# Performance work log

Hardware: AMD Instinct MI355X
Metric: run time of the kernel (lower is better)

The kernel has to match this reference:

```python
import jax, jax.numpy as jnp
import numpy as np

B, L, T, H = 8, 16, 1024, 256


def setup_inputs() -> dict:
    key = jax.random.key(0)
    k1, k2 = jax.random.split(key)
    h_blth = jax.random.normal(k1, (B, L, T, H), dtype=jnp.float32)
    # nn.Linear(H, 1): weight [1, H] -> store as [H]; bias [1]
    attn_w = jax.random.normal(k2, (H,), dtype=jnp.float32) / np.sqrt(H)
    attn_b = jnp.zeros((1,), dtype=jnp.float32)
    return {"h_blth": h_blth, "attn_w": attn_w, "attn_b": attn_b}


def reference(h_blth, attn_w, attn_b):
    # scores: [B, L, T]
    s = jnp.einsum('blth,h->blt', h_blth, attn_w) + attn_b[0]
    # global max over T (matches torch .max(dim=2, keepdim=True))
    s_max = jnp.max(s, axis=2, keepdims=True)
    exp_s = jnp.exp(s - s_max)                      # [B, L, T]
    cum_exp = jnp.cumsum(exp_s, axis=2)             # [B, L, T]
    weighted_h = exp_s[..., None] * h_blth          # [B, L, T, H]
    cum_weighted_h = jnp.cumsum(weighted_h, axis=2) # [B, L, T, H]
    ctx = cum_weighted_h / (cum_exp[..., None] + 1e-12)
    return h_blth + ctx
```

## Files before the change

### kernel.cpp

```cpp
#include <hip/hip_runtime.h>


constexpr int Tn = 1024, Hn = 256;
constexpr int BL  = 128;
constexpr int NCH = 8;
constexpr int CT  = Tn / NCH;
constexpr int F4  = Hn / 4;
constexpr int NW  = Tn / 32;

__global__ __launch_bounds__(256) void k_scores(const float* __restrict__ h,
                                                const float* __restrict__ w,
                                                const float* __restrict__ bias,
                                                float* __restrict__ ebuf,
                                                float* __restrict__ P32,
                                                float* __restrict__ Se32) {
    const int wave = threadIdx.x >> 6, lane = threadIdx.x & 63;
    const int g = lane >> 4, sub = lane & 15;
    const int j = blockIdx.x & 7, bl = blockIdx.x >> 3;
    const float b0 = bias[0];
    const float4* wp = reinterpret_cast<const float4*>(w);
    float4 w4[4];
    #pragma unroll
    for (int q = 0; q < 4; ++q) w4[q] = wp[sub + 16 * q];
    const float4* hp = reinterpret_cast<const float4*>(h) + (size_t)bl * Tn * F4;
    const int t0 = j * CT + wave * 32;

    float4 acc[4] = {{0,0,0,0},{0,0,0,0},{0,0,0,0},{0,0,0,0}};
    float esum = 0.f;
    #pragma unroll
    for (int i = 0; i < 8; ++i) {
        const int t = t0 + i * 4 + g;
        float4 x[4];
        #pragma unroll
        for (int q = 0; q < 4; ++q) x[q] = hp[(size_t)t * F4 + sub + 16 * q];
        float p = 0.f;
        #pragma unroll
        for (int q = 0; q < 4; ++q) {
            p = fmaf(x[q].x, w4[q].x, p);
            p = fmaf(x[q].y, w4[q].y, p);
            p = fmaf(x[q].z, w4[q].z, p);
            p = fmaf(x[q].w, w4[q].w, p);
        }
        p += __shfl_xor(p, 1);
        p += __shfl_xor(p, 2);
        p += __shfl_xor(p, 4);
        p += __shfl_xor(p, 8);
        const float e = __expf(p + b0);
        esum += e;
        #pragma unroll
        for (int q = 0; q < 4; ++q) {
            acc[q].x = fmaf(e, x[q].x, acc[q].x);
            acc[q].y = fmaf(e, x[q].y, acc[q].y);
            acc[q].z = fmaf(e, x[q].z, acc[q].z);
            acc[q].w = fmaf(e, x[q].w, acc[q].w);
        }
        if (sub == 0) ebuf[bl * Tn + t] = e;
    }
    #pragma unroll
    for (int q = 0; q < 4; ++q) {
        acc[q].x += __shfl_xor(acc[q].x, 16); acc[q].x += __shfl_xor(acc[q].x, 32);
        acc[q].y += __shfl_xor(acc[q].y, 16); acc[q].y += __shfl_xor(acc[q].y, 32);
        acc[q].z += __shfl_xor(acc[q].z, 16); acc[q].z += __shfl_xor(acc[q].z, 32);
        acc[q].w += __shfl_xor(acc[q].w, 16); acc[q].w += __shfl_xor(acc[q].w, 32);
    }
    esum += __shfl_xor(esum, 16);  esum += __shfl_xor(esum, 32);

    const int W = j * 4 + wave;
    if (lane < 16) {
        float4* pp = reinterpret_cast<float4*>(P32) + ((size_t)bl * NW + W) * F4;
        pp[sub]      = acc[0];
        pp[sub + 16] = acc[1];
        pp[sub + 32] = acc[2];
        pp[sub + 48] = acc[3];
    }
    if (lane == 0) Se32[bl * NW + W] = esum;
}

__global__ __launch_bounds__(256) void k_apply(const float* __restrict__ h,
                                               const float* __restrict__ ebuf,
                                               const float* __restrict__ P32,
                                               const float* __restrict__ Se32,
                                               float* __restrict__ out) {
    const int wave = threadIdx.x >> 6, lane = threadIdx.x & 63;
    const int j = blockIdx.x & 7, bl = blockIdx.x >> 3;
    const int W = j * 4 + wave;
    const int t0 = W * 32;

    const float4* Pp = reinterpret_cast<const float4*>(P32) + (size_t)bl * NW * F4;
    float4 off4 = make_float4(0.f, 0.f, 0.f, 0.f);
    for (int q = 0; q < W; ++q) {
        const float4 v = Pp[q * F4 + lane];
        off4.x += v.x; off4.y += v.y; off4.z += v.z; off4.w += v.w;
    }
    float seo = 0.f;
    if (lane < W) seo = Se32[bl * NW + lane];
    seo += __shfl_xor(seo, 1); seo += __shfl_xor(seo, 2);
    seo += __shfl_xor(seo, 4); seo += __shfl_xor(seo, 8);
    seo += __shfl_xor(seo, 16);
    seo = __shfl(seo, 0);

    float ev = 0.f;
    if (lane < 32) ev = ebuf[bl * Tn + t0 + lane];
    float sc = ev;
    #pragma unroll
    for (int off = 1; off < 32; off <<= 1) {
        const float n = __shfl_up(sc, off);
        if (lane >= off) sc += n;
    }
    const float sdv = 1.0f / (seo + sc + 1e-12f);

    const float4* hp = reinterpret_cast<const float4*>(h)
                       + ((size_t)bl * Tn + t0) * F4 + lane;
    float4* op = reinterpret_cast<float4*>(out)
                 + ((size_t)bl * Tn + t0) * F4 + lane;

    float4 a = off4;
    #pragma unroll
    for (int i = 0; i < 32; i += 8) {
        float4 x[8];
        #pragma unroll
        for (int u = 0; u < 8; ++u) x[u] = hp[(size_t)(i + u) * F4];
        #pragma unroll
        for (int u = 0; u < 8; ++u) {
            const float e = __shfl(ev,  i + u);
            const float s = __shfl(sdv, i + u);
            a.x = fmaf(e, x[u].x, a.x); a.y = fmaf(e, x[u].y, a.y);
            a.z = fmaf(e, x[u].z, a.z); a.w = fmaf(e, x[u].w, a.w);
            float4 o;
            o.x = fmaf(a.x, s, x[u].x); o.y = fmaf(a.y, s, x[u].y);
            o.z = fmaf(a.z, s, x[u].z); o.w = fmaf(a.w, s, x[u].w);
            op[(size_t)(i + u) * F4] = o;
        }
    }
}

extern "C" void kernel_launch(void* const* d_in, const int* in_sizes, int n_in,
                              void* d_out, int out_size, void* d_ws, size_t ws_size,
                              hipStream_t stream) {
    const float* h = (const float*)d_in[0];
    const float* w = (const float*)d_in[1];
    const float* b = (const float*)d_in[2];
    float* out = (float*)d_out;

    float* ebuf = (float*)d_ws;
    float* P32  = ebuf + BL * Tn;
    float* Se32 = P32 + (size_t)BL * NW * Hn;

    k_scores<<<BL * NCH, 256, 0, stream>>>(h, w, b, ebuf, P32, Se32);
    k_apply <<<BL * NCH, 256, 0, stream>>>(h, ebuf, P32, Se32, out);
}
```

Baseline: 262.0 us.

## Fuse score and apply kernels into one cooperative kernel with grid sync

Result: slower. 320.5 us (+22.3%).

```diff
diff --git a/kernel.cpp b/kernel.cpp
--- a/kernel.cpp
+++ b/kernel.cpp
@@ -1,45 +1,44 @@
 #include <hip/hip_runtime.h>
+#include <hip/hip_cooperative_groups.h>
+
+namespace cg = cooperative_groups;
 
 
 constexpr int Tn = 1024, Hn = 256;
 constexpr int BL  = 128;
 constexpr int NCH = 8;
-constexpr int CT  = Tn / NCH;
 constexpr int F4  = Hn / 4;
 constexpr int NW  = Tn / 32;
-
-__global__ __launch_bounds__(256) void k_scores(const float* __restrict__ h,
-                                                const float* __restrict__ w,
-                                                const float* __restrict__ bias,
-                                                float* __restrict__ ebuf,
-                                                float* __restrict__ P32,
-                                                float* __restrict__ Se32) {
-    const int wave = threadIdx.x >> 6, lane = threadIdx.x & 63;
-    const int g = lane >> 4, sub = lane & 15;
-    const int j = blockIdx.x & 7, bl = blockIdx.x >> 3;
-    const float b0 = bias[0];
-    const float4* wp = reinterpret_cast<const float4*>(w);
-    float4 w4[4];
-    #pragma unroll
-    for (int q = 0; q < 4; ++q) w4[q] = wp[sub + 16 * q];
+constexpr int NBLK = 512;
+constexpr int REP  = BL * NCH / NBLK;
+
+__device__ __forceinline__ void phase1_body(int vb, int wave, int lane,
+                                            int g, int sub, float b0,
+                                            const float4* __restrict__ wp4,
+                                            const float* __restrict__ h,
+                                            float* __restrict__ ebuf,
+                                            float* __restrict__ P32,
+                                            float* __restrict__ Se32) {
+    const int j = vb & 7, bl = vb >> 3;
+    const int W = j * 4 + wave;
+    const int t0w = W * 32;
     const float4* hp = reinterpret_cast<const float4*>(h) + (size_t)bl * Tn * F4;
-    const int t0 = j * CT + wave * 32;
 
     float4 acc[4] = {{0,0,0,0},{0,0,0,0},{0,0,0,0},{0,0,0,0}};
     float esum = 0.f;
     #pragma unroll
     for (int i = 0; i < 8; ++i) {
-        const int t = t0 + i * 4 + g;
+        const int t = t0w + i * 4 + g;
         float4 x[4];
         #pragma unroll
         for (int q = 0; q < 4; ++q) x[q] = hp[(size_t)t * F4 + sub + 16 * q];
         float p = 0.f;
         #pragma unroll
         for (int q = 0; q < 4; ++q) {
-            p = fmaf(x[q].x, w4[q].x, p);
-            p = fmaf(x[q].y, w4[q].y, p);
-            p = fmaf(x[q].z, w4[q].z, p);
-            p = fmaf(x[q].w, w4[q].w, p);
+            p = fmaf(x[q].x, wp4[q].x, p);
+            p = fmaf(x[q].y, wp4[q].y, p);
+            p = fmaf(x[q].z, wp4[q].z, p);
+            p = fmaf(x[q].w, wp4[q].w, p);
         }
         p += __shfl_xor(p, 1);
         p += __shfl_xor(p, 2);
@@ -65,7 +64,6 @@
     }
     esum += __shfl_xor(esum, 16);  esum += __shfl_xor(esum, 32);
 
-    const int W = j * 4 + wave;
     if (lane < 16) {
         float4* pp = reinterpret_cast<float4*>(P32) + ((size_t)bl * NW + W) * F4;
         pp[sub]      = acc[0];
@@ -76,15 +74,15 @@
     if (lane == 0) Se32[bl * NW + W] = esum;
 }
 
-__global__ __launch_bounds__(256) void k_apply(const float* __restrict__ h,
-                                               const float* __restrict__ ebuf,
-                                               const float* __restrict__ P32,
-                                               const float* __restrict__ Se32,
-                                               float* __restrict__ out) {
-    const int wave = threadIdx.x >> 6, lane = threadIdx.x & 63;
-    const int j = blockIdx.x & 7, bl = blockIdx.x >> 3;
+__device__ __forceinline__ void phase2_body(int vb, int wave, int lane,
+                                            const float* __restrict__ h,
+                                            const float* __restrict__ ebuf,
+                                            const float* __restrict__ P32,
+                                            const float* __restrict__ Se32,
+                                            float* __restrict__ out) {
+    const int j = vb & 7, bl = vb >> 3;
     const int W = j * 4 + wave;
-    const int t0 = W * 32;
+    const int t0w = W * 32;
 
     const float4* Pp = reinterpret_cast<const float4*>(P32) + (size_t)bl * NW * F4;
     float4 off4 = make_float4(0.f, 0.f, 0.f, 0.f);
@@ -100,7 +98,7 @@
     seo = __shfl(seo, 0);
 
     float ev = 0.f;
-    if (lane < 32) ev = ebuf[bl * Tn + t0 + lane];
+    if (lane < 32) ev = ebuf[bl * Tn + t0w + lane];
     float sc = ev;
     #pragma unroll
     for (int off = 1; off < 32; off <<= 1) {
@@ -110,9 +108,9 @@
     const float sdv = 1.0f / (seo + sc + 1e-12f);
 
     const float4* hp = reinterpret_cast<const float4*>(h)
-                       + ((size_t)bl * Tn + t0) * F4 + lane;
+                       + ((size_t)bl * Tn + t0w) * F4 + lane;
     float4* op = reinterpret_cast<float4*>(out)
-                 + ((size_t)bl * Tn + t0) * F4 + lane;
+                 + ((size_t)bl * Tn + t0w) * F4 + lane;
 
     float4 a = off4;
     #pragma unroll
@@ -134,6 +132,59 @@
     }
 }
 
+__global__ __launch_bounds__(256, 2) void k_coop(const float* __restrict__ h,
+                                                 const float* __restrict__ w,
+                                                 const float* __restrict__ bias,
+                                                 float* __restrict__ ebuf,
+                                                 float* __restrict__ P32,
+                                                 float* __restrict__ Se32,
+                                                 float* __restrict__ out) {
+    const int wave = threadIdx.x >> 6, lane = threadIdx.x & 63;
+    const int g = lane >> 4, sub = lane & 15;
+    const float b0 = bias[0];
+    const float4* wp = reinterpret_cast<const float4*>(w);
+    float4 w4[4];
+    #pragma unroll
+    for (int q = 0; q < 4; ++q) w4[q] = wp[sub + 16 * q];
+
+    #pragma unroll
+    for (int rep = 0; rep < REP; ++rep)
+        phase1_body(blockIdx.x + rep * NBLK, wave, lane, g, sub, b0, w4,
+                    h, ebuf, P32, Se32);
+
+    cg::this_grid().sync();
+
+    #pragma unroll
+    for (int rep = 0; rep < REP; ++rep)
+        phase2_body(blockIdx.x + rep * NBLK, wave, lane,
+                    h, ebuf, P32, Se32, out);
+}
+
+__global__ __launch_bounds__(256) void k_scores(const float* __restrict__ h,
+                                                const float* __restrict__ w,
+                                                const float* __restrict__ bias,
+                                                float* __restrict__ ebuf,
+                                                float* __restrict__ P32,
+                                                float* __restrict__ Se32) {
+    const int wave = threadIdx.x >> 6, lane = threadIdx.x & 63;
+    const int g = lane >> 4, sub = lane & 15;
+    const float b0 = bias[0];
+    const float4* wp = reinterpret_cast<const float4*>(w);
+    float4 w4[4];
+    #pragma unroll
+    for (int q = 0; q < 4; ++q) w4[q] = wp[sub + 16 * q];
+    phase1_body(blockIdx.x, wave, lane, g, sub, b0, w4, h, ebuf, P32, Se32);
+}
+
+__global__ __launch_bounds__(256) void k_apply(const float* __restrict__ h,
+                                               const float* __restrict__ ebuf,
+                                               const float* __restrict__ P32,
+                                               const float* __restrict__ Se32,
+                                               float* __restrict__ out) {
+    const int wave = threadIdx.x >> 6, lane = threadIdx.x & 63;
+    phase2_body(blockIdx.x, wave, lane, h, ebuf, P32, Se32, out);
+}
+
 extern "C" void kernel_launch(void* const* d_in, const int* in_sizes, int n_in,
                               void* d_out, int out_size, void* d_ws, size_t ws_size,
                               hipStream_t stream) {
@@ -146,6 +197,14 @@
     float* P32  = ebuf + BL * Tn;
     float* Se32 = P32 + (size_t)BL * NW * Hn;
 
-    k_scores<<<BL * NCH, 256, 0, stream>>>(h, w, b, ebuf, P32, Se32);
-    k_apply <<<BL * NCH, 256, 0, stream>>>(h, ebuf, P32, Se32, out);
-}
+    void* args[] = {(void*)&h, (void*)&w, (void*)&b,
+                    (void*)&ebuf, (void*)&P32, (void*)&Se32, (void*)&out};
+    hipError_t err = hipLaunchCooperativeKernel(reinterpret_cast<void*>(k_coop),
+                                                dim3(NBLK), dim3(256), args, 0,
+                                                stream);
+    if (err != hipSuccess) {
+        (void)hipGetLastError();
+        k_scores<<<BL * NCH, 256, 0, stream>>>(h, w, b, ebuf, P32, Se32);
+        k_apply <<<BL * NCH, 256, 0, stream>>>(h, ebuf, P32, Se32, out);
+    }
+}
```
